# Kernel tuning notes

Measured on AMD Instinct MI355X. Metric: run time of the kernel, lower is better.

Reference implementation:

```python
import jax, jax.numpy as jnp
import numpy as np

N, D, K = 131072, 64, 1024


def setup_inputs() -> dict:
    key = jax.random.key(0)
    kx, kc = jax.random.split(key)
    x = jax.random.normal(kx, (N, D), dtype=jnp.float32)
    # codebook ~ trunc_normal(std=0.2); plain normal*0.2 is a faithful stand-in
    codebook = 0.2 * jax.random.normal(kc, (K, D), dtype=jnp.float32)
    temperature = jnp.ones((1,), dtype=jnp.float32)
    return {"x": x, "codebook": codebook, "temperature": temperature}


def reference(x, codebook, temperature):
    # squared euclidean distances: [N, K]
    dist = (
        jnp.sum(x * x, axis=1, keepdims=True)
        + jnp.sum(codebook * codebook, axis=1)[None, :]
        - 2.0 * (x @ codebook.T)
    )
    neg_dist = -dist
    ids = jnp.argmax(neg_dist, axis=1)  # nearest code per row
    # Note: original tests `if self.train:` (a bound method, always truthy),
    # so the gumbel-softmax branch always executes.
    gkey = jax.random.key(42)
    g = jax.random.gumbel(gkey, neg_dist.shape, dtype=neg_dist.dtype)
    weights = jax.nn.softmax((neg_dist + g) / temperature[0], axis=-1)  # [N, K]
    emb = weights @ codebook  # [N, D]
    return emb, ids
```

## Files before the change

### kernel.cpp

```cpp
#include <hip/hip_runtime.h>
#include <stdint.h>

#define N_ROWS 131072
#define DIM 64
#define K_CODES 1024

typedef __attribute__((ext_vector_type(8))) short short8;
typedef __attribute__((ext_vector_type(4))) float float4v;
typedef __attribute__((ext_vector_type(4))) uint32_t u32x4;

__device__ __forceinline__ uint32_t cvt_pk_bf16(float lo, float hi) {
    uint32_t r;
    asm("v_cvt_pk_bf16_f32 %0, %1, %2" : "=v"(r) : "v"(lo), "v"(hi));
    return r;
}
__device__ __forceinline__ uint32_t lo_pack(float fe, float fo, uint32_t h) {
    float le = fe - __uint_as_float(h << 16);
    float lo_ = fo - __uint_as_float(h & 0xffff0000u);
    return cvt_pk_bf16(le, lo_);
}

__device__ __forceinline__ void dma16(const void* g, void* l) {
    __builtin_amdgcn_global_load_lds(
        (const __attribute__((address_space(1))) uint32_t*)g,
        (__attribute__((address_space(3))) uint32_t*)l,
        16, 0, 0);
}

template<int V> struct IC { static constexpr int v = V; };

__global__ __launch_bounds__(256) void sumc2_kernel(const float* __restrict__ cb,
                                                    float* __restrict__ sumc2) {
    int k = blockIdx.x * 256 + threadIdx.x;
    if (k < K_CODES) {
        const float* r = cb + k * DIM;
        float s = 0.f;
        #pragma unroll
        for (int j = 0; j < DIM; ++j) s = fmaf(r[j], r[j], s);
        sumc2[k] = s;
    }
}

__global__ __launch_bounds__(256) void cbimg_kernel(const float* __restrict__ cb,
                                                    uint16_t* __restrict__ img) {
    const int tile = blockIdx.x, tid = threadIdx.x;
    const int code = tid & 31, db = (tid >> 5) * 8;
    const int k = tile * 32 + code;
    const float4* src = reinterpret_cast<const float4*>(cb + (size_t)k * DIM + db);
    const float4 a = src[0], b = src[1];
    uint32_t h0 = cvt_pk_bf16(a.x, a.y), h1 = cvt_pk_bf16(a.z, a.w);
    uint32_t h2 = cvt_pk_bf16(b.x, b.y), h3 = cvt_pk_bf16(b.z, b.w);
    u32x4 hv = {h0, h1, h2, h3};
    u32x4 lv = { lo_pack(a.x,a.y,h0), lo_pack(a.z,a.w,h1),
                 lo_pack(b.x,b.y,h2), lo_pack(b.z,b.w,h3) };
    uint16_t* t = img + (size_t)tile * 7168;
    *(u32x4*)&t[code*72 + db]        = hv;
    *(u32x4*)&t[2304 + code*72 + db] = lv;
    const int pc = ((code & 15) << 1) | (code >> 4);
    t[4608 + (db+0)*40 + pc] = (uint16_t)h0;
    t[4608 + (db+1)*40 + pc] = (uint16_t)(h0 >> 16);
    t[4608 + (db+2)*40 + pc] = (uint16_t)h1;
    t[4608 + (db+3)*40 + pc] = (uint16_t)(h1 >> 16);
    t[4608 + (db+4)*40 + pc] = (uint16_t)h2;
    t[4608 + (db+5)*40 + pc] = (uint16_t)(h2 >> 16);
    t[4608 + (db+6)*40 + pc] = (uint16_t)h3;
    t[4608 + (db+7)*40 + pc] = (uint16_t)(h3 >> 16);
}

__device__ __forceinline__ uint32_t rotl32(uint32_t x, uint32_t r) {
    return (x << r) | (x >> (32u - r));
}
__device__ __forceinline__ void tf_round(uint32_t& x0, uint32_t& x1, uint32_t r) {
    x0 += x1; x1 = rotl32(x1, r); x1 ^= x0;
}
__device__ __forceinline__ void threefry2x32_k42(uint32_t c0, uint32_t c1,
                                                 uint32_t& o0, uint32_t& o1) {
    const uint32_t ks0 = 0u, ks1 = 42u, ks2 = 0x1BD11BDAu ^ 0u ^ 42u;
    uint32_t x0 = c0 + ks0, x1 = c1 + ks1;
    tf_round(x0,x1,13); tf_round(x0,x1,15); tf_round(x0,x1,26); tf_round(x0,x1,6);
    x0 += ks1; x1 += ks2 + 1u;
    tf_round(x0,x1,17); tf_round(x0,x1,29); tf_round(x0,x1,16); tf_round(x0,x1,24);
    x0 += ks2; x1 += ks0 + 2u;
    tf_round(x0,x1,13); tf_round(x0,x1,15); tf_round(x0,x1,26); tf_round(x0,x1,6);
    x0 += ks0; x1 += ks1 + 3u;
    tf_round(x0,x1,17); tf_round(x0,x1,29); tf_round(x0,x1,16); tf_round(x0,x1,24);
    x0 += ks1; x1 += ks2 + 4u;
    tf_round(x0,x1,13); tf_round(x0,x1,15); tf_round(x0,x1,26); tf_round(x0,x1,6);
    x0 += ks2; x1 += ks0 + 5u;
    o0 = x0; o1 = x1;
}

__device__ __forceinline__ float gumbel_v(uint32_t bits) {
    uint32_t fb = (bits >> 9) | 0x3f800000u;
    float f = __uint_as_float(fb) - 1.0f;
    float u = fmaxf(1.17549435e-38f, f);
    float w = u - 1.0f;
    float p = fmaf(w, 0.2f, -0.25f);
    p = fmaf(w, p, 0.33333333333f);
    p = fmaf(w, p, -0.5f);
    p = fmaf(w, p, 1.0f);
    float v_poly = -(w * p);
    float v_log  = -__logf(u);
    return (u > 0.9375f) ? v_poly : v_log;
}

template<bool T1>
__device__ __forceinline__ void quant_body(
    const float* __restrict__ x, const uint16_t* __restrict__ img,
    const float* __restrict__ cb, const float* __restrict__ sumc2g,
    const float invT, float* __restrict__ out_emb, float* __restrict__ out_ids,
    char* smem)
{
    uint16_t* const xhiP  = (uint16_t*)smem;
    uint16_t* const xloP  = (uint16_t*)(smem + 9216);
    uint16_t* const pbufP = (uint16_t*)(smem + 28672);

    const int tid  = threadIdx.x;
    const int wave = tid >> 6, lane = tid & 63, quad = lane >> 4, col = lane & 15;
    const int rowbase = blockIdx.x * 32 + wave * 8;
    const float twoi = 2.0f * invT;

    {
        const int s = tid >> 2, w = s >> 4, t = s & 15, dq = tid & 3;
        const int row = blockIdx.x * 32 + w * 8 + (t >> 1) + ((t & 1) << 16);
        const float4* src = reinterpret_cast<const float4*>(x + (size_t)row * DIM + dq * 16);
        float4 f0 = src[0], f1 = src[1], f2 = src[2], f3 = src[3];
        u32x4 hA = { cvt_pk_bf16(f0.x,f0.y), cvt_pk_bf16(f0.z,f0.w),
                     cvt_pk_bf16(f1.x,f1.y), cvt_pk_bf16(f1.z,f1.w) };
        u32x4 hB = { cvt_pk_bf16(f2.x,f2.y), cvt_pk_bf16(f2.z,f2.w),
                     cvt_pk_bf16(f3.x,f3.y), cvt_pk_bf16(f3.z,f3.w) };
        u32x4 lA = { lo_pack(f0.x,f0.y,hA[0]), lo_pack(f0.z,f0.w,hA[1]),
                     lo_pack(f1.x,f1.y,hA[2]), lo_pack(f1.z,f1.w,hA[3]) };
        u32x4 lB = { lo_pack(f2.x,f2.y,hB[0]), lo_pack(f2.z,f2.w,hB[1]),
                     lo_pack(f3.x,f3.y,hB[2]), lo_pack(f3.z,f3.w,hB[3]) };
        uint16_t* dsth = &xhiP[(w*16 + t)*72 + dq*16];
        uint16_t* dstl = &xloP[(w*16 + t)*72 + dq*16];
        *(u32x4*)(dsth)     = hA;
        *(u32x4*)(dsth + 8) = hB;
        *(u32x4*)(dstl)     = lA;
        *(u32x4*)(dstl + 8) = lB;
    }
    __syncthreads();

    const int arb = (wave*16 + col)*72;
    const short8 ahi0 = *(const short8*)&xhiP[arb + quad*8];
    const short8 ahi1 = *(const short8*)&xhiP[arb + 32 + quad*8];
    const short8 alo0 = *(const short8*)&xloP[arb + quad*8];
    const short8 alo1 = *(const short8*)&xloP[arb + 32 + quad*8];
    __syncthreads();

    const char* gdma = (const char*)img + (size_t)lane * 16;
    auto dma_tile = [&](int tile, int bofs) {
        const char* s = gdma + (size_t)tile * 14336;
        char* d = smem + bofs;
        dma16(s + (size_t)wave*1024,     d + wave*1024);
        dma16(s + (size_t)(wave+4)*1024, d + (wave+4)*1024);
        dma16(s + (size_t)(wave+8)*1024, d + (wave+8)*1024);
        if (wave < 2) dma16(s + (size_t)(wave+12)*1024, d + (wave+12)*1024);
    };
    dma_tile(0, 0);
    __syncthreads();

    float m[4]  = {-1e30f, -1e30f, -1e30f, -1e30f};
    float Zp[4] = {0.f, 0.f, 0.f, 0.f};
    float4v e0 = {0,0,0,0}, e1 = {0,0,0,0}, e2 = {0,0,0,0}, e3 = {0,0,0,0};
    float zt[4] = {-3.4e38f,-3.4e38f,-3.4e38f,-3.4e38f};
    float zs[4] = {-3.4e38f,-3.4e38f,-3.4e38f,-3.4e38f};
    int   kt[4] = {0,0,0,0}, ks[4] = {0,0,0,0};

    const uint32_t base_c0 = (uint32_t)(rowbase + 2*quad) * 1024u + (uint32_t)col;

    auto body = [&](int blk, auto B) {
        constexpr int BOF = decltype(B)::v;
        const uint16_t* cbhi = (const uint16_t*)(smem + BOF);
        const uint16_t* cblo = cbhi + 2304;
        const uint16_t* cbT  = cbhi + 4608;
        const int kb  = blk * 32;
        const int kc0 = kb + col, kc1 = kc0 + 16;

        if (blk + 1 < 32) dma_tile(blk + 1, BOF ^ 14336);

        const float sc0 = sumc2g[kc0], sc1 = sumc2g[kc1];

        float v0[4], v1[4];
        {
            uint32_t o0, o1;
            const uint32_t cA = base_c0 + (uint32_t)kb;
            threefry2x32_k42(cA,         cA + (1u<<26),          o0, o1);
            v0[0] = gumbel_v(o0); v0[1] = gumbel_v(o1);
            threefry2x32_k42(cA + 1024u, cA + 1024u + (1u<<26),  o0, o1);
            v0[2] = gumbel_v(o0); v0[3] = gumbel_v(o1);
            threefry2x32_k42(cA + 16u,   cA + 16u + (1u<<26),    o0, o1);
            v1[0] = gumbel_v(o0); v1[1] = gumbel_v(o1);
            threefry2x32_k42(cA + 1040u, cA + 1040u + (1u<<26),  o0, o1);
            v1[2] = gumbel_v(o0); v1[3] = gumbel_v(o1);
        }
        float r0[4], r1[4];
        #pragma unroll
        for (int j = 0; j < 4; ++j) {
            if (T1) { r0[j] = __builtin_amdgcn_rcpf(v0[j]); r1[j] = __builtin_amdgcn_rcpf(v1[j]); }
            else    { r0[j] = -invT * __logf(v0[j]);        r1[j] = -invT * __logf(v1[j]); }
        }

        float4v S0 = {0,0,0,0}, S1 = {0,0,0,0};
        {
            const int rb0 = col*72;
            const short8 bh0 = *(const short8*)&cbhi[rb0 + quad*8];
            const short8 bh1 = *(const short8*)&cbhi[rb0 + 32 + quad*8];
            const short8 bl0 = *(const short8*)&cblo[rb0 + quad*8];
            const short8 bl1 = *(const short8*)&cblo[rb0 + 32 + quad*8];
            S0 = __builtin_amdgcn_mfma_f32_16x16x32_bf16(ahi0, bh0, S0, 0,0,0);
            S0 = __builtin_amdgcn_mfma_f32_16x16x32_bf16(ahi1, bh1, S0, 0,0,0);
            S0 = __builtin_amdgcn_mfma_f32_16x16x32_bf16(ahi0, bl0, S0, 0,0,0);
            S0 = __builtin_amdgcn_mfma_f32_16x16x32_bf16(ahi1, bl1, S0, 0,0,0);
            S0 = __builtin_amdgcn_mfma_f32_16x16x32_bf16(alo0, bh0, S0, 0,0,0);
            S0 = __builtin_amdgcn_mfma_f32_16x16x32_bf16(alo1, bh1, S0, 0,0,0);
        }
        {
            const int rb1 = (16 + col)*72;
            const short8 bh0 = *(const short8*)&cbhi[rb1 + quad*8];
            const short8 bh1 = *(const short8*)&cbhi[rb1 + 32 + quad*8];
            const short8 bl0 = *(const short8*)&cblo[rb1 + quad*8];
            const short8 bl1 = *(const short8*)&cblo[rb1 + 32 + quad*8];
            S1 = __builtin_amdgcn_mfma_f32_16x16x32_bf16(ahi0, bh0, S1, 0,0,0);
            S1 = __builtin_amdgcn_mfma_f32_16x16x32_bf16(ahi1, bh1, S1, 0,0,0);
            S1 = __builtin_amdgcn_mfma_f32_16x16x32_bf16(ahi0, bl0, S1, 0,0,0);
            S1 = __builtin_amdgcn_mfma_f32_16x16x32_bf16(ahi1, bl1, S1, 0,0,0);
            S1 = __builtin_amdgcn_mfma_f32_16x16x32_bf16(alo0, bh0, S1, 0,0,0);
            S1 = __builtin_amdgcn_mfma_f32_16x16x32_bf16(alo1, bh1, S1, 0,0,0);
        }

        const float nsc0 = -invT * sc0, nsc1 = -invT * sc1;
        float a0[4], a1[4], zm[4];
        #pragma unroll
        for (int j = 0; j < 4; ++j) {
            const float z0 = fmaf(S0[j], twoi, nsc0);
            const float z1 = fmaf(S1[j], twoi, nsc1);
            {   const bool c1 = z0 > zt[j], c2 = z0 > zs[j];
                const float zsn = __builtin_amdgcn_fmed3f(z0, zt[j], zs[j]);
                ks[j] = c1 ? kt[j] : (c2 ? kc0 : ks[j]);
                kt[j] = c1 ? kc0 : kt[j];
                zt[j] = fmaxf(zt[j], z0);
                zs[j] = zsn; }
            {   const bool c1 = z1 > zt[j], c2 = z1 > zs[j];
                const float zsn = __builtin_amdgcn_fmed3f(z1, zt[j], zs[j]);
                ks[j] = c1 ? kt[j] : (c2 ? kc1 : ks[j]);
                kt[j] = c1 ? kc1 : kt[j];
                zt[j] = fmaxf(zt[j], z1);
                zs[j] = zsn; }
            a0[j] = T1 ? z0 : (z0 + r0[j]);
            a1[j] = T1 ? z1 : (z1 + r1[j]);
            zm[j] = fmaxf(a0[j], a1[j]);
        }

        bool need;
        if (T1) {
            const float dm = fmaxf(fmaxf(zm[0]-m[0], zm[1]-m[1]), fmaxf(zm[2]-m[2], zm[3]-m[3]));
            need = __any(dm > 11.0f);
        } else need = true;
        if (need) {
            float4v av;
            #pragma unroll
            for (int j = 0; j < 4; ++j) {
                float mn = fmaxf(m[j], zm[j]);
                #pragma unroll
                for (int mask = 1; mask < 16; mask <<= 1)
                    mn = fmaxf(mn, __shfl_xor(mn, mask));
                const float al = __expf(m[j] - mn);
                m[j] = mn; Zp[j] *= al; av[j] = al;
            }
            e0 *= av; e1 *= av; e2 *= av; e3 *= av;
        }

        #pragma unroll
        for (int j = 0; j < 4; ++j) {
            float p0 = __expf(a0[j] - m[j]);
            float p1 = __expf(a1[j] - m[j]);
            if (T1) { p0 *= r0[j]; p1 *= r1[j]; }
            Zp[j] += p0 + p1;
            ((uint32_t*)pbufP)[(wave*16 + quad*4 + j)*20 + col] = cvt_pk_bf16(p0, p1);
        }

        const short8 pa  = *(const short8*)&pbufP[(wave*16 + col)*40 + quad*8];
        const short8 bt0 = *(const short8*)&cbT[( 0 + col)*40 + quad*8];
        const short8 bt1 = *(const short8*)&cbT[(16 + col)*40 + quad*8];
        const short8 bt2 = *(const short8*)&cbT[(32 + col)*40 + quad*8];
        const short8 bt3 = *(const short8*)&cbT[(48 + col)*40 + quad*8];
        e0 = __builtin_amdgcn_mfma_f32_16x16x32_bf16(pa, bt0, e0, 0,0,0);
        e1 = __builtin_amdgcn_mfma_f32_16x16x32_bf16(pa, bt1, e1, 0,0,0);
        e2 = __builtin_amdgcn_mfma_f32_16x16x32_bf16(pa, bt2, e2, 0,0,0);
        e3 = __builtin_amdgcn_mfma_f32_16x16x32_bf16(pa, bt3, e3, 0,0,0);

        __syncthreads();
    };

    for (int blk = 0; blk < 32; blk += 2) {
        body(blk,     IC<0>{});
        body(blk + 1, IC<14336>{});
    }

    #pragma unroll
    for (int mask = 1; mask < 16; mask <<= 1) {
        #pragma unroll
        for (int j = 0; j < 4; ++j) Zp[j] += __shfl_xor(Zp[j], mask);
    }
    #pragma unroll
    for (int mask = 1; mask < 16; mask <<= 1) {
        #pragma unroll
        for (int j = 0; j < 4; ++j) {
            const float ozt = __shfl_xor(zt[j], mask);
            const float ozs = __shfl_xor(zs[j], mask);
            const int   okt = __shfl_xor(kt[j], mask);
            const int   oks = __shfl_xor(ks[j], mask);
            const bool mf = (zt[j] > ozt) || (zt[j] == ozt && kt[j] < okt);
            const float w1 = mf ? zt[j] : ozt;  const int wk1 = mf ? kt[j] : okt;
            const float l1 = mf ? ozt : zt[j];  const int lk1 = mf ? okt : kt[j];
            const float w2 = mf ? zs[j] : ozs;  const int wk2 = mf ? ks[j] : oks;
            const bool s1 = (l1 > w2) || (l1 == w2 && lk1 < wk2);
            zt[j] = w1; kt[j] = wk1;
            zs[j] = s1 ? l1 : w2; ks[j] = s1 ? lk1 : wk2;
        }
    }
    if (col == 0) {
        #pragma unroll
        for (int j = 0; j < 4; ++j) {
            if (zt[j] - zs[j] < 1e-2f * invT) {
                const int t = quad*4 + j;
                const int row = rowbase + (t >> 1) + ((t & 1) << 16);
                const float* xr = x + (size_t)row * DIM;
                const float* cA = cb + (size_t)kt[j] * DIM;
                const float* cB = cb + (size_t)ks[j] * DIM;
                double dA = 0.0, dB = 0.0;
                for (int d = 0; d < DIM; ++d) {
                    const double xv = (double)xr[d];
                    const double av2 = (double)cA[d], bv = (double)cB[d];
                    dA = fma(av2, av2, dA); dA = fma(-2.0*xv, av2, dA);
                    dB = fma(bv,  bv,  dB); dB = fma(-2.0*xv, bv,  dB);
                }
                if (dB < dA || (dB == dA && ks[j] < kt[j])) kt[j] = ks[j];
            }
        }
    }
    #pragma unroll
    for (int j = 0; j < 4; ++j) {
        const int t = quad*4 + j;
        const int row = rowbase + (t >> 1) + ((t & 1) << 16);
        const float rZ = __builtin_amdgcn_rcpf(Zp[j]);
        out_emb[(size_t)row * DIM +      col] = e0[j] * rZ;
        out_emb[(size_t)row * DIM + 16 + col] = e1[j] * rZ;
        out_emb[(size_t)row * DIM + 32 + col] = e2[j] * rZ;
        out_emb[(size_t)row * DIM + 48 + col] = e3[j] * rZ;
        if (col == 0) out_ids[row] = (float)kt[j];
    }
}

__global__ __launch_bounds__(256) __attribute__((amdgpu_waves_per_eu(4)))
void quant_kernel(
    const float* __restrict__ x, const uint16_t* __restrict__ img,
    const float* __restrict__ cb, const float* __restrict__ temp,
    const float* __restrict__ sumc2g,
    float* __restrict__ out_emb, float* __restrict__ out_ids)
{
    __shared__ __align__(16) char smem[33792];
    const float invT = 1.0f / temp[0];
    if (invT == 1.0f) quant_body<true >(x, img, cb, sumc2g, invT, out_emb, out_ids, smem);
    else              quant_body<false>(x, img, cb, sumc2g, invT, out_emb, out_ids, smem);
}

extern "C" void kernel_launch(void* const* d_in, const int* in_sizes, int n_in,
                              void* d_out, int out_size, void* d_ws, size_t ws_size,
                              hipStream_t stream) {
    const float* x    = (const float*)d_in[0];
    const float* cb   = (const float*)d_in[1];
    const float* temp = (const float*)d_in[2];
    float*    sumc2   = (float*)d_ws;
    uint16_t* img     = (uint16_t*)((char*)d_ws + 4096);
    float* out_emb    = (float*)d_out;
    float* out_ids    = (float*)d_out + (size_t)N_ROWS * DIM;

    sumc2_kernel<<<(K_CODES + 255) / 256, 256, 0, stream>>>(cb, sumc2);
    cbimg_kernel<<<32, 256, 0, stream>>>(cb, img);
    quant_kernel<<<N_ROWS / 64, 256, 0, stream>>>(x, img, cb, temp, sumc2, out_emb, out_ids);
}
```

Measured before the change: 361.2 us.

## Software-pipeline Gumbel RNG one tile ahead and switch softmax to base-2 exponentials

Computes the threefry/Gumbel noise for the next codebook tile while the current tile's MFMAs are in flight, interleaving four threefry streams for ILP. Distance-MFMA chains for the two code halves are interleaved to overlap dependent accumulations. Scales are folded into log2e so raw v_exp_f32/v_log_f32 replace __expf/__logf, and the rescale threshold and near-tie refinement margin are adjusted to match the base-2 scaling. This adds register pressure from holding next-iteration noise and computes one extra RNG batch past the end.

```diff
diff --git a/kernel.cpp b/kernel.cpp
--- a/kernel.cpp
+++ b/kernel.cpp
@@ -18,6 +18,12 @@
     float le = fe - __uint_as_float(h << 16);
     float lo_ = fo - __uint_as_float(h & 0xffff0000u);
     return cvt_pk_bf16(le, lo_);
+}
+__device__ __forceinline__ float exp2_fast(float x) {
+    float r; asm("v_exp_f32 %0, %1" : "=v"(r) : "v"(x)); return r;
+}
+__device__ __forceinline__ float log2_fast(float x) {
+    float r; asm("v_log_f32 %0, %1" : "=v"(r) : "v"(x)); return r;
 }
 
 __device__ __forceinline__ void dma16(const void* g, void* l) {
@@ -70,24 +76,31 @@
 __device__ __forceinline__ uint32_t rotl32(uint32_t x, uint32_t r) {
     return (x << r) | (x >> (32u - r));
 }
-__device__ __forceinline__ void tf_round(uint32_t& x0, uint32_t& x1, uint32_t r) {
-    x0 += x1; x1 = rotl32(x1, r); x1 ^= x0;
-}
-__device__ __forceinline__ void threefry2x32_k42(uint32_t c0, uint32_t c1,
-                                                 uint32_t& o0, uint32_t& o1) {
-    const uint32_t ks0 = 0u, ks1 = 42u, ks2 = 0x1BD11BDAu ^ 0u ^ 42u;
-    uint32_t x0 = c0 + ks0, x1 = c1 + ks1;
-    tf_round(x0,x1,13); tf_round(x0,x1,15); tf_round(x0,x1,26); tf_round(x0,x1,6);
-    x0 += ks1; x1 += ks2 + 1u;
-    tf_round(x0,x1,17); tf_round(x0,x1,29); tf_round(x0,x1,16); tf_round(x0,x1,24);
-    x0 += ks2; x1 += ks0 + 2u;
-    tf_round(x0,x1,13); tf_round(x0,x1,15); tf_round(x0,x1,26); tf_round(x0,x1,6);
-    x0 += ks0; x1 += ks1 + 3u;
-    tf_round(x0,x1,17); tf_round(x0,x1,29); tf_round(x0,x1,16); tf_round(x0,x1,24);
-    x0 += ks1; x1 += ks2 + 4u;
-    tf_round(x0,x1,13); tf_round(x0,x1,15); tf_round(x0,x1,26); tf_round(x0,x1,6);
-    x0 += ks2; x1 += ks0 + 5u;
-    o0 = x0; o1 = x1;
+__device__ __forceinline__ void tf_round4(uint32_t x0[4], uint32_t x1[4], uint32_t r) {
+    #pragma unroll
+    for (int i = 0; i < 4; ++i) { x0[i] += x1[i]; x1[i] = rotl32(x1[i], r); x1[i] ^= x0[i]; }
+}
+__device__ __forceinline__ void threefry4w_k42(const uint32_t c0[4],
+                                               uint32_t o0[4], uint32_t o1[4]) {
+    const uint32_t ks1 = 42u, ks2 = 0x1BD11BDAu ^ 42u;
+    uint32_t x0[4], x1[4];
+    #pragma unroll
+    for (int i = 0; i < 4; ++i) { x0[i] = c0[i]; x1[i] = c0[i] + (1u<<26) + ks1; }
+    tf_round4(x0,x1,13); tf_round4(x0,x1,15); tf_round4(x0,x1,26); tf_round4(x0,x1,6);
+    #pragma unroll
+    for (int i = 0; i < 4; ++i) { x0[i] += ks1; x1[i] += ks2 + 1u; }
+    tf_round4(x0,x1,17); tf_round4(x0,x1,29); tf_round4(x0,x1,16); tf_round4(x0,x1,24);
+    #pragma unroll
+    for (int i = 0; i < 4; ++i) { x0[i] += ks2; x1[i] += 2u; }
+    tf_round4(x0,x1,13); tf_round4(x0,x1,15); tf_round4(x0,x1,26); tf_round4(x0,x1,6);
+    #pragma unroll
+    for (int i = 0; i < 4; ++i) { x1[i] += ks1 + 3u; }
+    tf_round4(x0,x1,17); tf_round4(x0,x1,29); tf_round4(x0,x1,16); tf_round4(x0,x1,24);
+    #pragma unroll
+    for (int i = 0; i < 4; ++i) { x0[i] += ks1; x1[i] += ks2 + 4u; }
+    tf_round4(x0,x1,13); tf_round4(x0,x1,15); tf_round4(x0,x1,26); tf_round4(x0,x1,6);
+    #pragma unroll
+    for (int i = 0; i < 4; ++i) { o0[i] = x0[i] + ks2; o1[i] = x1[i] + 5u; }
 }
 
 __device__ __forceinline__ float gumbel_v(uint32_t bits) {
@@ -104,6 +117,8 @@
     return (u > 0.9375f) ? v_poly : v_log;
 }
 
+#define LOG2E 1.4426950408889634f
+
 template<bool T1>
 __device__ __forceinline__ void quant_body(
     const float* __restrict__ x, const uint16_t* __restrict__ img,
@@ -118,7 +133,8 @@
     const int tid  = threadIdx.x;
     const int wave = tid >> 6, lane = tid & 63, quad = lane >> 4, col = lane & 15;
     const int rowbase = blockIdx.x * 32 + wave * 8;
-    const float twoi = 2.0f * invT;
+    const float twoi = 2.0f * invT * LOG2E;
+    const float cnsc = -invT * LOG2E;
 
     {
         const int s = tid >> 2, w = s >> 4, t = s & 15, dq = tid & 3;
@@ -158,7 +174,27 @@
         dma16(s + (size_t)(wave+8)*1024, d + (wave+8)*1024);
         if (wave < 2) dma16(s + (size_t)(wave+12)*1024, d + (wave+12)*1024);
     };
+
+    const uint32_t base_c0 = (uint32_t)(rowbase + 2*quad) * 1024u + (uint32_t)col;
+
+    auto rng_iter = [&](int blk, float* r0, float* r1) {
+        const uint32_t cA = base_c0 + (uint32_t)(blk * 32);
+        const uint32_t c0s[4] = {cA, cA + 1024u, cA + 16u, cA + 1040u};
+        uint32_t o0[4], o1[4];
+        threefry4w_k42(c0s, o0, o1);
+        float v[8];
+        #pragma unroll
+        for (int i = 0; i < 4; ++i) { v[2*i] = gumbel_v(o0[i]); v[2*i+1] = gumbel_v(o1[i]); }
+        #pragma unroll
+        for (int j = 0; j < 4; ++j) {
+            if (T1) { r0[j] = __builtin_amdgcn_rcpf(v[j]);  r1[j] = __builtin_amdgcn_rcpf(v[4+j]); }
+            else    { r0[j] = -invT * log2_fast(v[j]);      r1[j] = -invT * log2_fast(v[4+j]); }
+        }
+    };
+
     dma_tile(0, 0);
+    float r0c[4], r1c[4];
+    rng_iter(0, r0c, r1c);
     __syncthreads();
 
     float m[4]  = {-1e30f, -1e30f, -1e30f, -1e30f};
@@ -167,8 +203,6 @@
     float zt[4] = {-3.4e38f,-3.4e38f,-3.4e38f,-3.4e38f};
     float zs[4] = {-3.4e38f,-3.4e38f,-3.4e38f,-3.4e38f};
     int   kt[4] = {0,0,0,0}, ks[4] = {0,0,0,0};
-
-    const uint32_t base_c0 = (uint32_t)(rowbase + 2*quad) * 1024u + (uint32_t)col;
 
     auto body = [&](int blk, auto B) {
         constexpr int BOF = decltype(B)::v;
@@ -179,58 +213,35 @@
         const int kc0 = kb + col, kc1 = kc0 + 16;
 
         if (blk + 1 < 32) dma_tile(blk + 1, BOF ^ 14336);
-
         const float sc0 = sumc2g[kc0], sc1 = sumc2g[kc1];
 
-        float v0[4], v1[4];
-        {
-            uint32_t o0, o1;
-            const uint32_t cA = base_c0 + (uint32_t)kb;
-            threefry2x32_k42(cA,         cA + (1u<<26),          o0, o1);
-            v0[0] = gumbel_v(o0); v0[1] = gumbel_v(o1);
-            threefry2x32_k42(cA + 1024u, cA + 1024u + (1u<<26),  o0, o1);
-            v0[2] = gumbel_v(o0); v0[3] = gumbel_v(o1);
-            threefry2x32_k42(cA + 16u,   cA + 16u + (1u<<26),    o0, o1);
-            v1[0] = gumbel_v(o0); v1[1] = gumbel_v(o1);
-            threefry2x32_k42(cA + 1040u, cA + 1040u + (1u<<26),  o0, o1);
-            v1[2] = gumbel_v(o0); v1[3] = gumbel_v(o1);
-        }
-        float r0[4], r1[4];
-        #pragma unroll
-        for (int j = 0; j < 4; ++j) {
-            if (T1) { r0[j] = __builtin_amdgcn_rcpf(v0[j]); r1[j] = __builtin_amdgcn_rcpf(v1[j]); }
-            else    { r0[j] = -invT * __logf(v0[j]);        r1[j] = -invT * __logf(v1[j]); }
-        }
-
         float4v S0 = {0,0,0,0}, S1 = {0,0,0,0};
-        {
-            const int rb0 = col*72;
-            const short8 bh0 = *(const short8*)&cbhi[rb0 + quad*8];
-            const short8 bh1 = *(const short8*)&cbhi[rb0 + 32 + quad*8];
-            const short8 bl0 = *(const short8*)&cblo[rb0 + quad*8];
-            const short8 bl1 = *(const short8*)&cblo[rb0 + 32 + quad*8];
-            S0 = __builtin_amdgcn_mfma_f32_16x16x32_bf16(ahi0, bh0, S0, 0,0,0);
-            S0 = __builtin_amdgcn_mfma_f32_16x16x32_bf16(ahi1, bh1, S0, 0,0,0);
-            S0 = __builtin_amdgcn_mfma_f32_16x16x32_bf16(ahi0, bl0, S0, 0,0,0);
-            S0 = __builtin_amdgcn_mfma_f32_16x16x32_bf16(ahi1, bl1, S0, 0,0,0);
-            S0 = __builtin_amdgcn_mfma_f32_16x16x32_bf16(alo0, bh0, S0, 0,0,0);
-            S0 = __builtin_amdgcn_mfma_f32_16x16x32_bf16(alo1, bh1, S0, 0,0,0);
-        }
-        {
-            const int rb1 = (16 + col)*72;
-            const short8 bh0 = *(const short8*)&cbhi[rb1 + quad*8];
-            const short8 bh1 = *(const short8*)&cbhi[rb1 + 32 + quad*8];
-            const short8 bl0 = *(const short8*)&cblo[rb1 + quad*8];
-            const short8 bl1 = *(const short8*)&cblo[rb1 + 32 + quad*8];
-            S1 = __builtin_amdgcn_mfma_f32_16x16x32_bf16(ahi0, bh0, S1, 0,0,0);
-            S1 = __builtin_amdgcn_mfma_f32_16x16x32_bf16(ahi1, bh1, S1, 0,0,0);
-            S1 = __builtin_amdgcn_mfma_f32_16x16x32_bf16(ahi0, bl0, S1, 0,0,0);
-            S1 = __builtin_amdgcn_mfma_f32_16x16x32_bf16(ahi1, bl1, S1, 0,0,0);
-            S1 = __builtin_amdgcn_mfma_f32_16x16x32_bf16(alo0, bh0, S1, 0,0,0);
-            S1 = __builtin_amdgcn_mfma_f32_16x16x32_bf16(alo1, bh1, S1, 0,0,0);
-        }
-
-        const float nsc0 = -invT * sc0, nsc1 = -invT * sc1;
+        const int rb0 = col*72, rb1 = (16 + col)*72;
+        const short8 b0h0 = *(const short8*)&cbhi[rb0 + quad*8];
+        const short8 b0h1 = *(const short8*)&cbhi[rb0 + 32 + quad*8];
+        const short8 b0l0 = *(const short8*)&cblo[rb0 + quad*8];
+        const short8 b0l1 = *(const short8*)&cblo[rb0 + 32 + quad*8];
+        const short8 b1h0 = *(const short8*)&cbhi[rb1 + quad*8];
+        const short8 b1h1 = *(const short8*)&cbhi[rb1 + 32 + quad*8];
+        const short8 b1l0 = *(const short8*)&cblo[rb1 + quad*8];
+        const short8 b1l1 = *(const short8*)&cblo[rb1 + 32 + quad*8];
+        S0 = __builtin_amdgcn_mfma_f32_16x16x32_bf16(ahi0, b0h0, S0, 0,0,0);
+        S1 = __builtin_amdgcn_mfma_f32_16x16x32_bf16(ahi0, b1h0, S1, 0,0,0);
+        S0 = __builtin_amdgcn_mfma_f32_16x16x32_bf16(ahi1, b0h1, S0, 0,0,0);
+        S1 = __builtin_amdgcn_mfma_f32_16x16x32_bf16(ahi1, b1h1, S1, 0,0,0);
+        S0 = __builtin_amdgcn_mfma_f32_16x16x32_bf16(ahi0, b0l0, S0, 0,0,0);
+        S1 = __builtin_amdgcn_mfma_f32_16x16x32_bf16(ahi0, b1l0, S1, 0,0,0);
+        S0 = __builtin_amdgcn_mfma_f32_16x16x32_bf16(ahi1, b0l1, S0, 0,0,0);
+        S1 = __builtin_amdgcn_mfma_f32_16x16x32_bf16(ahi1, b1l1, S1, 0,0,0);
+        S0 = __builtin_amdgcn_mfma_f32_16x16x32_bf16(alo0, b0h0, S0, 0,0,0);
+        S1 = __builtin_amdgcn_mfma_f32_16x16x32_bf16(alo0, b1h0, S1, 0,0,0);
+        S0 = __builtin_amdgcn_mfma_f32_16x16x32_bf16(alo1, b0h1, S0, 0,0,0);
+        S1 = __builtin_amdgcn_mfma_f32_16x16x32_bf16(alo1, b1h1, S1, 0,0,0);
+
+        float nr0[4], nr1[4];
+        rng_iter(blk + 1, nr0, nr1);
+
+        const float nsc0 = cnsc * sc0, nsc1 = cnsc * sc1;
         float a0[4], a1[4], zm[4];
         #pragma unroll
         for (int j = 0; j < 4; ++j) {
@@ -248,15 +259,15 @@
                 kt[j] = c1 ? kc1 : kt[j];
                 zt[j] = fmaxf(zt[j], z1);
                 zs[j] = zsn; }
-            a0[j] = T1 ? z0 : (z0 + r0[j]);
-            a1[j] = T1 ? z1 : (z1 + r1[j]);
+            a0[j] = T1 ? z0 : (z0 + r0c[j]);
+            a1[j] = T1 ? z1 : (z1 + r1c[j]);
             zm[j] = fmaxf(a0[j], a1[j]);
         }
 
         bool need;
         if (T1) {
             const float dm = fmaxf(fmaxf(zm[0]-m[0], zm[1]-m[1]), fmaxf(zm[2]-m[2], zm[3]-m[3]));
-            need = __any(dm > 11.0f);
+            need = __any(dm > 15.0f);
         } else need = true;
         if (need) {
             float4v av;
@@ -266,7 +277,7 @@
                 #pragma unroll
                 for (int mask = 1; mask < 16; mask <<= 1)
                     mn = fmaxf(mn, __shfl_xor(mn, mask));
-                const float al = __expf(m[j] - mn);
+                const float al = exp2_fast(m[j] - mn);
                 m[j] = mn; Zp[j] *= al; av[j] = al;
             }
             e0 *= av; e1 *= av; e2 *= av; e3 *= av;
@@ -274,9 +285,9 @@
 
         #pragma unroll
         for (int j = 0; j < 4; ++j) {
-            float p0 = __expf(a0[j] - m[j]);
-            float p1 = __expf(a1[j] - m[j]);
-            if (T1) { p0 *= r0[j]; p1 *= r1[j]; }
+            float p0 = exp2_fast(a0[j] - m[j]);
+            float p1 = exp2_fast(a1[j] - m[j]);
+            if (T1) { p0 *= r0c[j]; p1 *= r1c[j]; }
             Zp[j] += p0 + p1;
             ((uint32_t*)pbufP)[(wave*16 + quad*4 + j)*20 + col] = cvt_pk_bf16(p0, p1);
         }
@@ -292,6 +303,9 @@
         e3 = __builtin_amdgcn_mfma_f32_16x16x32_bf16(pa, bt3, e3, 0,0,0);
 
         __syncthreads();
+
+        #pragma unroll
+        for (int i = 0; i < 4; ++i) { r0c[i] = nr0[i]; r1c[i] = nr1[i]; }
     };
 
     for (int blk = 0; blk < 32; blk += 2) {
@@ -324,7 +338,7 @@
     if (col == 0) {
         #pragma unroll
         for (int j = 0; j < 4; ++j) {
-            if (zt[j] - zs[j] < 1e-2f * invT) {
+            if (zt[j] - zs[j] < 0.015f * invT) {
                 const int t = quad*4 + j;
                 const int row = rowbase + (t >> 1) + ((t & 1) << 16);
                 const float* xr = x + (size_t)row * DIM;
```

Result: slower. 501.5 us (+38.9%).
